# Optimization experiments

Measured on AMD Instinct MI355X. Metric: run time of the kernel, lower is better.

The kernel has to match this reference:

```python
import jax, jax.numpy as jnp
import numpy as np

N_NODES = 100000
N_EDGES = 3200000
N_RELS = 8
F_IN = 64
F_OUT = 64


def setup_inputs() -> dict:
    key = jax.random.key(0)
    k1, k2, k3, k4, k5, k6 = jax.random.split(key, 6)
    X = jax.random.normal(k1, (N_NODES, F_IN), dtype=jnp.float32)
    W = jax.random.normal(k2, (N_RELS, F_IN, F_OUT), dtype=jnp.float32) * 0.1
    A = jax.random.uniform(k3, (N_EDGES,), dtype=jnp.float32)
    src = jax.random.randint(k4, (N_EDGES,), 0, N_NODES, dtype=jnp.int32)
    dst = jax.random.randint(k5, (N_EDGES,), 0, N_NODES, dtype=jnp.int32)
    etype = jax.random.randint(k6, (N_EDGES,), 0, N_RELS, dtype=jnp.int32)
    return {"X": X, "W": W, "A": A, "src": src, "dst": dst, "etype": etype}


def reference(X, W, A, src, dst, etype):
    # RGCN hetero forward: Y[i,fo] = sum_{r,j in N_r(i)} A[r,i,j] * (X[j] @ W[r])[fo]
    # Precompute per-relation transformed features: [R, N, F_out]
    XW = jnp.einsum('nf,rfo->rno', X, W)
    # Gather per-edge message and scale by edge weight: [E, F_out]
    msg = XW[etype, src] * A[:, None]
    # Scatter-add into destination nodes: [N, F_out]
    Y = jax.ops.segment_sum(msg, dst, num_segments=X.shape[0])
    return Y
```

## Files before the change

### kernel.cpp

```cpp
#include <hip/hip_runtime.h>
#include <hip/hip_fp16.h>

#define FDIM 64
#define SB 200
#define P_BLK 1024
#define NB_MAX 400
#define BKT_NODES 256

typedef __attribute__((ext_vector_type(8))) short short8;
typedef __attribute__((ext_vector_type(4))) float float4_;

__device__ __forceinline__ unsigned short f2bf(float x) {
    unsigned u = __float_as_uint(x);
    return (unsigned short)((u + 0x7FFF + ((u >> 16) & 1)) >> 16);
}

__global__ __launch_bounds__(256) void xw_gemm_mfma(
    const float* __restrict__ X, const float* __restrict__ Wmat,
    __half* __restrict__ XWh, int N, int R)
{
    __shared__ unsigned short Wt[4 * 64 * 72];
    const int tid  = threadIdx.x;
    const int lane = tid & 63;
    const int wave = tid >> 6;
    const int quad = lane >> 4;
    const int l15  = lane & 15;
    const int blockBase = blockIdx.x * 256;

    short8 bfrag[4][2];
    bool tvalid[4];
#pragma unroll
    for (int t = 0; t < 4; ++t) {
        const int tb = blockBase + (wave * 4 + t) * 16;
        tvalid[t] = (tb < N);
        if (tvalid[t]) {
            const float* xp = X + (size_t)(tb + l15) * FDIM + quad * 8;
            const float4 x0 = *(const float4*)(xp);
            const float4 x1 = *(const float4*)(xp + 4);
            const float4 x2 = *(const float4*)(xp + 32);
            const float4 x3 = *(const float4*)(xp + 36);
            short8 b0, b1;
            b0[0]=f2bf(x0.x); b0[1]=f2bf(x0.y); b0[2]=f2bf(x0.z); b0[3]=f2bf(x0.w);
            b0[4]=f2bf(x1.x); b0[5]=f2bf(x1.y); b0[6]=f2bf(x1.z); b0[7]=f2bf(x1.w);
            b1[0]=f2bf(x2.x); b1[1]=f2bf(x2.y); b1[2]=f2bf(x2.z); b1[3]=f2bf(x2.w);
            b1[4]=f2bf(x3.x); b1[5]=f2bf(x3.y); b1[6]=f2bf(x3.z); b1[7]=f2bf(x3.w);
            bfrag[t][0] = b0; bfrag[t][1] = b1;
        } else {
            bfrag[t][0] = (short8)(0); bfrag[t][1] = (short8)(0);
        }
    }

    for (int rp = 0; rp < 2; ++rp) {
        __syncthreads();
#pragma unroll
        for (int it = 0; it < 16; ++it) {
            const int idx = it * 256 + tid;
            const int k  = idx & 63;
            const int f4 = (idx >> 6) & 15;
            const int r  = idx >> 10;
            const float4 w = *(const float4*)(Wmat + (((size_t)(rp * 4 + r) * FDIM + k) * FDIM + f4 * 4));
            const int base = (r * 64 + f4 * 4) * 72 + k;
            Wt[base + 0 * 72] = f2bf(w.x);
            Wt[base + 1 * 72] = f2bf(w.y);
            Wt[base + 2 * 72] = f2bf(w.z);
            Wt[base + 3 * 72] = f2bf(w.w);
        }
        __syncthreads();

#pragma unroll
        for (int t = 0; t < 4; ++t) {
            if (!tvalid[t]) continue;
            const int tb = blockBase + (wave * 4 + t) * 16;
            const int node = tb + l15;
#pragma unroll
            for (int r = 0; r < 4; ++r) {
                __half* orow = XWh + ((size_t)(rp * 4 + r) * N + node) * FDIM;
#pragma unroll
                for (int ft = 0; ft < 4; ++ft) {
                    const int f = ft * 16 + l15;
                    const unsigned short* wp = &Wt[(r * 64 + f) * 72 + quad * 8];
                    const short8 a0 = *(const short8*)(wp);
                    const short8 a1 = *(const short8*)(wp + 32);
                    float4_ acc = {0.f, 0.f, 0.f, 0.f};
                    acc = __builtin_amdgcn_mfma_f32_16x16x32_bf16(a0, bfrag[t][0], acc, 0, 0, 0);
                    acc = __builtin_amdgcn_mfma_f32_16x16x32_bf16(a1, bfrag[t][1], acc, 0, 0, 0);
                    const __half2 h01 = __floats2half2_rn(acc[0], acc[1]);
                    const __half2 h23 = __floats2half2_rn(acc[2], acc[3]);
                    uint2 st;
                    st.x = *(const unsigned*)&h01;
                    st.y = *(const unsigned*)&h23;
                    *(uint2*)(orow + ft * 16 + quad * 4) = st;
                }
            }
        }
    }
}

__global__ __launch_bounds__(256) void bin_hist(
    const int* __restrict__ dst, int* __restrict__ cnt, int E, int B, int chunk)
{
    __shared__ int lh[NB_MAX];
    const int p = blockIdx.x, tid = threadIdx.x;
    for (int b = tid; b < B; b += 256) lh[b] = 0;
    __syncthreads();
    const int i0 = p * chunk, iend = min(i0 + chunk, E);
    for (int i = i0 + tid; i < iend; i += 256)
        atomicAdd(&lh[dst[i] >> 8], 1);
    __syncthreads();
    for (int b = tid; b < B; b += 256) cnt[(size_t)b * P_BLK + p] = lh[b];
}

__global__ __launch_bounds__(256) void scan_partial(
    const int* __restrict__ cnt, int* __restrict__ blockSums, int M, int CH)
{
    __shared__ int sh[256];
    const int b = blockIdx.x, tid = threadIdx.x;
    const int i0 = b * CH, iend = min(i0 + CH, M);
    int s = 0;
    for (int i = i0 + tid; i < iend; i += 256) s += cnt[i];
    sh[tid] = s; __syncthreads();
    for (int off = 128; off > 0; off >>= 1) {
        if (tid < off) sh[tid] += sh[tid + off];
        __syncthreads();
    }
    if (tid == 0) blockSums[b] = sh[0];
}

__global__ __launch_bounds__(256) void scan_block(int* blockSums, int nb)
{
    __shared__ int sh[256];
    const int tid = threadIdx.x;
    const int v = (tid < nb) ? blockSums[tid] : 0;
    sh[tid] = v; __syncthreads();
    for (int off = 1; off < 256; off <<= 1) {
        const int t = (tid >= off) ? sh[tid - off] : 0;
        __syncthreads();
        sh[tid] += t;
        __syncthreads();
    }
    if (tid < nb) blockSums[tid] = sh[tid] - v;
}

__global__ __launch_bounds__(64) void scan_final(
    const int* __restrict__ cnt, const int* __restrict__ blockSums,
    int* __restrict__ offs, int M, int CH, int E)
{
    const int b = blockIdx.x, lane = threadIdx.x;
    const int i0 = b * CH, iend = min(i0 + CH, M);
    int carry = blockSums[b];
    for (int t = i0; t < iend; t += 64) {
        const int i = t + lane;
        const int c = (i < iend) ? cnt[i] : 0;
        int v = c;
#pragma unroll
        for (int o = 1; o < 64; o <<= 1) {
            const int u = __shfl_up(v, o, 64);
            if (lane >= o) v += u;
        }
        if (i < iend) offs[i] = carry + v - c;
        carry += __shfl(v, 63, 64);
    }
    if (b == (int)gridDim.x - 1 && lane == 0) offs[M] = E;
}

__global__ __launch_bounds__(256) void bin_scatter(
    const int* __restrict__ src, const int* __restrict__ dst,
    const int* __restrict__ etype, const float* __restrict__ A,
    const int* __restrict__ offs, int2* __restrict__ packed,
    int E, int N, int B, int chunk)
{
    __shared__ int lcur[NB_MAX];
    const int p = blockIdx.x, tid = threadIdx.x;
    for (int b = tid; b < B; b += 256) lcur[b] = offs[(size_t)b * P_BLK + p];
    __syncthreads();
    const int i0 = p * chunk, iend = min(i0 + chunk, E);
    for (int i = i0 + tid; i < iend; i += 256) {
        const int d = dst[i];
        const int b = d >> 8;
        const int pos = atomicAdd(&lcur[b], 1);
        const int lo = (etype[i] * N + src[i]) | ((d & (BKT_NODES - 1)) << 20);
        packed[pos] = make_int2(lo, __float_as_int(A[i]));
    }
}

__global__ __launch_bounds__(256) void bucket_sort(
    const int2* __restrict__ packed, const int* __restrict__ offs,
    int2* __restrict__ sorted, int* __restrict__ nodeOffs, int N, int B, int E)
{
    __shared__ int hist[BKT_NODES];
    __shared__ int pfx[BKT_NODES + 1];
    __shared__ int cur[BKT_NODES];
    const int bkt = blockIdx.x, tid = threadIdx.x;
    const int beg = offs[(size_t)bkt * P_BLK];
    const int end = (bkt + 1 < B) ? offs[(size_t)(bkt + 1) * P_BLK] : E;

    hist[tid] = 0;
    __syncthreads();
    for (int i = beg + tid; i < end; i += 256)
        atomicAdd(&hist[(packed[i].x >> 20) & (BKT_NODES - 1)], 1);
    __syncthreads();
    if (tid == 0) {
        int s = 0;
        pfx[0] = 0;
        for (int i = 0; i < BKT_NODES; ++i) { s += hist[i]; pfx[i + 1] = s; }
    }
    __syncthreads();
    {
        cur[tid] = pfx[tid];
        const int n = bkt * BKT_NODES + tid;
        if (n < N) nodeOffs[n] = beg + pfx[tid];
    }
    if (bkt == B - 1 && tid == 0) nodeOffs[N] = E;
    __syncthreads();
    for (int i = beg + tid; i < end; i += 256) {
        const int2 rec = packed[i];
        const int d = (rec.x >> 20) & (BKT_NODES - 1);
        const int pos = atomicAdd(&cur[d], 1);
        sorted[beg + pos] = rec;
    }
}

__global__ __launch_bounds__(256) void dst_aggregate(
    const __half* __restrict__ XWh, const int* __restrict__ nodeOffs,
    const int2* __restrict__ sorted, float* __restrict__ Y, int N)
{
    const int lane = threadIdx.x & 63;
    const int hid  = lane >> 5;
    const int fl   = lane & 31;
    const int wave = (int)((blockIdx.x * blockDim.x + threadIdx.x) >> 6);
    const int nWaves = (int)((gridDim.x * blockDim.x) >> 6);
    const __half2* XW2 = (const __half2*)XWh;

    for (int d = wave; d < N; d += nWaves) {
        const int beg = nodeOffs[d], end = nodeOffs[d + 1];
        float ax = 0.f, ay = 0.f;
        for (int base = beg; base < end; base += 64) {
            const int idx = base + lane;
            const int2 ka = (idx < end) ? sorted[idx] : make_int2(0, 0);
            const int nb = min(64, end - base);
            const int npair = (nb + 1) >> 1;
            int s = 0;
            for (; s + 8 <= npair; s += 8) {
                int k[8], b[8];
#pragma unroll
                for (int u = 0; u < 8; ++u) {
                    const int j = 2 * (s + u) + hid;
                    k[u] = __shfl(ka.x, j, 64);
                    b[u] = __shfl(ka.y, j, 64);
                }
                __half2 v[8];
#pragma unroll
                for (int u = 0; u < 8; ++u)
                    v[u] = XW2[(size_t)(k[u] & 0xFFFFF) * 32 + fl];
#pragma unroll
                for (int u = 0; u < 8; ++u) {
                    const float2 f = __half22float2(v[u]);
                    const float a = __int_as_float(b[u]);
                    ax += a * f.x; ay += a * f.y;
                }
            }
            for (; s < npair; ++s) {
                const int j = 2 * s + hid;
                const int kk = __shfl(ka.x, j, 64);
                const int bb = __shfl(ka.y, j, 64);
                const __half2 v = XW2[(size_t)(kk & 0xFFFFF) * 32 + fl];
                const float2 f = __half22float2(v);
                const float a = __int_as_float(bb);
                ax += a * f.x; ay += a * f.y;
            }
        }
        ax += __shfl_xor(ax, 32, 64);
        ay += __shfl_xor(ay, 32, 64);
        if (lane < 32) {
            ((float2*)(Y + (size_t)d * FDIM))[fl] = make_float2(ax, ay);
        }
    }
}

extern "C" void kernel_launch(void* const* d_in, const int* in_sizes, int n_in,
                              void* d_out, int out_size, void* d_ws, size_t ws_size,
                              hipStream_t stream)
{
    const float* X     = (const float*)d_in[0];
    const float* Wmat  = (const float*)d_in[1];
    const float* A     = (const float*)d_in[2];
    const int*   src   = (const int*)d_in[3];
    const int*   dst   = (const int*)d_in[4];
    const int*   etype = (const int*)d_in[5];
    float* Y = (float*)d_out;

    const int N = in_sizes[0] / FDIM;
    const int R = in_sizes[1] / (FDIM * FDIM);
    const int E = in_sizes[2];
    (void)n_in; (void)out_size; (void)ws_size;

    const int B = (N + BKT_NODES - 1) / BKT_NODES;
    const int M = B * P_BLK;
    const int chunk = (E + P_BLK - 1) / P_BLK;
    const int CH = (M + SB - 1) / SB;

    char* ws = (char*)d_ws;
    size_t off = 0;
    auto take = [&](size_t bytes) { char* p = ws + off; off = (off + bytes + 255) & ~(size_t)255; return p; };
    __half* XWh      = (__half*)take((size_t)R * N * FDIM * sizeof(__half));
    int2*   packed   = (int2*)  take((size_t)E * sizeof(int2));
    int2*   sorted   = (int2*)  take((size_t)E * sizeof(int2));
    int*    cnt      = (int*)   take((size_t)M * sizeof(int));
    int*    offs     = (int*)   take((size_t)(M + 1) * sizeof(int));
    int*    nodeOffs = (int*)   take((size_t)(N + 1) * sizeof(int));
    int*    bsums    = (int*)   take((size_t)SB * sizeof(int));

    xw_gemm_mfma<<<(N + 255) / 256, 256, 0, stream>>>(X, Wmat, XWh, N, R);

    bin_hist<<<P_BLK, 256, 0, stream>>>(dst, cnt, E, B, chunk);
    scan_partial<<<SB, 256, 0, stream>>>(cnt, bsums, M, CH);
    scan_block<<<1, 256, 0, stream>>>(bsums, SB);
    scan_final<<<SB, 64, 0, stream>>>(cnt, bsums, offs, M, CH, E);
    bin_scatter<<<P_BLK, 256, 0, stream>>>(src, dst, etype, A, offs, packed, E, N, B, chunk);
    bucket_sort<<<B, 256, 0, stream>>>(packed, offs, sorted, nodeOffs, N, B, E);

    dst_aggregate<<<2048, 256, 0, stream>>>(XWh, nodeOffs, sorted, Y, N);
}
```

Before: 358.7 us.

## Stage bin scatter through LDS and precompute per-node offsets via global histogram

The bin histogram now also counts edges per destination node with global atomics, and a second scan over those counts yields node offsets directly. Bucket sort therefore drops its histogram and serial prefix pass and runs with 1024 threads. Bin scatter does a local count and prefix, stages records in LDS grouped by bucket, and then writes them out contiguously, so global stores coalesce instead of scattering. The cost is 3.2M global atomics on node counts, three extra scan launches, a memset, and about 32KB of LDS per block in bin scatter, which lowers occupancy and requires each chunk to fit CHUNK_CAP.

After: 440.2 us. 1.23x slower.

```diff
diff --git a/kernel.cpp b/kernel.cpp
--- a/kernel.cpp
+++ b/kernel.cpp
@@ -6,6 +6,7 @@
 #define P_BLK 1024
 #define NB_MAX 400
 #define BKT_NODES 256
+#define CHUNK_CAP 3200
 
 typedef __attribute__((ext_vector_type(8))) short short8;
 typedef __attribute__((ext_vector_type(4))) float float4_;
@@ -97,15 +98,19 @@
 }
 
 __global__ __launch_bounds__(256) void bin_hist(
-    const int* __restrict__ dst, int* __restrict__ cnt, int E, int B, int chunk)
+    const int* __restrict__ dst, int* __restrict__ cnt,
+    int* __restrict__ nodeCnt, int E, int B, int chunk)
 {
     __shared__ int lh[NB_MAX];
     const int p = blockIdx.x, tid = threadIdx.x;
     for (int b = tid; b < B; b += 256) lh[b] = 0;
     __syncthreads();
     const int i0 = p * chunk, iend = min(i0 + chunk, E);
-    for (int i = i0 + tid; i < iend; i += 256)
-        atomicAdd(&lh[dst[i] >> 8], 1);
+    for (int i = i0 + tid; i < iend; i += 256) {
+        const int d = dst[i];
+        atomicAdd(&lh[d >> 8], 1);
+        atomicAdd(&nodeCnt[d], 1);
+    }
     __syncthreads();
     for (int b = tid; b < B; b += 256) cnt[(size_t)b * P_BLK + p] = lh[b];
 }
@@ -169,54 +174,76 @@
     const int* __restrict__ offs, int2* __restrict__ packed,
     int E, int N, int B, int chunk)
 {
-    __shared__ int lcur[NB_MAX];
+    __shared__ int lcnt[NB_MAX];
+    __shared__ int lpfx[NB_MAX];
+    __shared__ int gb[NB_MAX];
+    __shared__ int2 recs[CHUNK_CAP];
+    __shared__ unsigned short rbkt[CHUNK_CAP];
     const int p = blockIdx.x, tid = threadIdx.x;
-    for (int b = tid; b < B; b += 256) lcur[b] = offs[(size_t)b * P_BLK + p];
-    __syncthreads();
     const int i0 = p * chunk, iend = min(i0 + chunk, E);
+
+    for (int b = tid; b < B; b += 256) lcnt[b] = 0;
+    __syncthreads();
+    for (int i = i0 + tid; i < iend; i += 256)
+        atomicAdd(&lcnt[dst[i] >> 8], 1);
+    __syncthreads();
+
+    if (tid < 64) {
+        int carry = 0;
+        for (int t0 = 0; t0 < B; t0 += 64) {
+            const int b = t0 + tid;
+            const int c = (b < B) ? lcnt[b] : 0;
+            int v = c;
+#pragma unroll
+            for (int o = 1; o < 64; o <<= 1) {
+                const int u = __shfl_up(v, o, 64);
+                if (tid >= o) v += u;
+            }
+            if (b < B) lpfx[b] = carry + v - c;
+            carry += __shfl(v, 63, 64);
+        }
+    }
+    __syncthreads();
+    for (int b = tid; b < B; b += 256) {
+        gb[b] = offs[(size_t)b * P_BLK + p] - lpfx[b];
+        lcnt[b] = lpfx[b];
+    }
+    __syncthreads();
+
     for (int i = i0 + tid; i < iend; i += 256) {
         const int d = dst[i];
         const int b = d >> 8;
-        const int pos = atomicAdd(&lcur[b], 1);
-        const int lo = (etype[i] * N + src[i]) | ((d & (BKT_NODES - 1)) << 20);
-        packed[pos] = make_int2(lo, __float_as_int(A[i]));
-    }
-}
-
-__global__ __launch_bounds__(256) void bucket_sort(
+        const int slot = atomicAdd(&lcnt[b], 1);
+        recs[slot] = make_int2((etype[i] * N + src[i]) | ((d & 255) << 20),
+                               __float_as_int(A[i]));
+        rbkt[slot] = (unsigned short)b;
+    }
+    __syncthreads();
+
+    const int tot = iend - i0;
+    for (int s = tid; s < tot; s += 256)
+        packed[gb[rbkt[s]] + s] = recs[s];
+}
+
+__global__ __launch_bounds__(1024) void bucket_sort(
     const int2* __restrict__ packed, const int* __restrict__ offs,
-    int2* __restrict__ sorted, int* __restrict__ nodeOffs, int N, int B, int E)
-{
-    __shared__ int hist[BKT_NODES];
-    __shared__ int pfx[BKT_NODES + 1];
+    const int* __restrict__ nodeOffs, int2* __restrict__ sorted,
+    int N, int B, int E)
+{
     __shared__ int cur[BKT_NODES];
     const int bkt = blockIdx.x, tid = threadIdx.x;
+    if (tid < BKT_NODES) {
+        const int n = bkt * BKT_NODES + tid;
+        cur[tid] = (n < N) ? nodeOffs[n] : E;
+    }
+    __syncthreads();
     const int beg = offs[(size_t)bkt * P_BLK];
     const int end = (bkt + 1 < B) ? offs[(size_t)(bkt + 1) * P_BLK] : E;
-
-    hist[tid] = 0;
-    __syncthreads();
-    for (int i = beg + tid; i < end; i += 256)
-        atomicAdd(&hist[(packed[i].x >> 20) & (BKT_NODES - 1)], 1);
-    __syncthreads();
-    if (tid == 0) {
-        int s = 0;
-        pfx[0] = 0;
-        for (int i = 0; i < BKT_NODES; ++i) { s += hist[i]; pfx[i + 1] = s; }
-    }
-    __syncthreads();
-    {
-        cur[tid] = pfx[tid];
-        const int n = bkt * BKT_NODES + tid;
-        if (n < N) nodeOffs[n] = beg + pfx[tid];
-    }
-    if (bkt == B - 1 && tid == 0) nodeOffs[N] = E;
-    __syncthreads();
-    for (int i = beg + tid; i < end; i += 256) {
+    for (int i = beg + tid; i < end; i += 1024) {
         const int2 rec = packed[i];
-        const int d = (rec.x >> 20) & (BKT_NODES - 1);
-        const int pos = atomicAdd(&cur[d], 1);
-        sorted[beg + pos] = rec;
+        const int dl = (rec.x >> 20) & (BKT_NODES - 1);
+        const int pos = atomicAdd(&cur[dl], 1);
+        sorted[pos] = rec;
     }
 }
 
@@ -297,7 +324,8 @@
     const int B = (N + BKT_NODES - 1) / BKT_NODES;
     const int M = B * P_BLK;
     const int chunk = (E + P_BLK - 1) / P_BLK;
-    const int CH = (M + SB - 1) / SB;
+    const int CH  = (M + SB - 1) / SB;
+    const int CH2 = (N + SB - 1) / SB;
 
     char* ws = (char*)d_ws;
     size_t off = 0;
@@ -307,17 +335,27 @@
     int2*   sorted   = (int2*)  take((size_t)E * sizeof(int2));
     int*    cnt      = (int*)   take((size_t)M * sizeof(int));
     int*    offs     = (int*)   take((size_t)(M + 1) * sizeof(int));
+    int*    nodeCnt  = (int*)   take((size_t)N * sizeof(int));
     int*    nodeOffs = (int*)   take((size_t)(N + 1) * sizeof(int));
     int*    bsums    = (int*)   take((size_t)SB * sizeof(int));
+    int*    bsums2   = (int*)   take((size_t)SB * sizeof(int));
+
+    hipMemsetAsync(nodeCnt, 0, (size_t)N * sizeof(int), stream);
 
     xw_gemm_mfma<<<(N + 255) / 256, 256, 0, stream>>>(X, Wmat, XWh, N, R);
 
-    bin_hist<<<P_BLK, 256, 0, stream>>>(dst, cnt, E, B, chunk);
+    bin_hist<<<P_BLK, 256, 0, stream>>>(dst, cnt, nodeCnt, E, B, chunk);
+
     scan_partial<<<SB, 256, 0, stream>>>(cnt, bsums, M, CH);
     scan_block<<<1, 256, 0, stream>>>(bsums, SB);
     scan_final<<<SB, 64, 0, stream>>>(cnt, bsums, offs, M, CH, E);
+
+    scan_partial<<<SB, 256, 0, stream>>>(nodeCnt, bsums2, N, CH2);
+    scan_block<<<1, 256, 0, stream>>>(bsums2, SB);
+    scan_final<<<SB, 64, 0, stream>>>(nodeCnt, bsums2, nodeOffs, N, CH2, E);
+
     bin_scatter<<<P_BLK, 256, 0, stream>>>(src, dst, etype, A, offs, packed, E, N, B, chunk);
-    bucket_sort<<<B, 256, 0, stream>>>(packed, offs, sorted, nodeOffs, N, B, E);
+    bucket_sort<<<B, 1024, 0, stream>>>(packed, offs, nodeOffs, sorted, N, B, E);
 
     dst_aggregate<<<2048, 256, 0, stream>>>(XWh, nodeOffs, sorted, Y, N);
 }
```
